# Optimization experiments

Measured on AMD Instinct MI355X. Metric: run time of the kernel, lower is better.

Reference implementation:

```python
import jax, jax.numpy as jnp
import numpy as np

N = 100000
E = 1600000
F_IN = 256   # 4 * 64 after concat
H = 128

def _glorot(key, shape):
    fan_in, fan_out = shape
    lim = jnp.sqrt(6.0 / (fan_in + fan_out))
    return jax.random.uniform(key, shape, jnp.float32, -lim, lim)

def setup_inputs() -> dict:
    key = jax.random.key(0)
    ks = jax.random.split(key, 32)
    inp = {
        'x': jax.random.normal(ks[0], (N, 64), jnp.float32),
        'diff': jax.random.normal(ks[1], (N, 64), jnp.float32),
        'rec_prev': jax.random.normal(ks[2], (N, 64), jnp.float32),
        'hidden_prev': jax.random.normal(ks[3], (N, 64), jnp.float32),
        'edge_index': jax.random.randint(ks[4], (2, E), 0, N, jnp.int64),
    }
    dims = [(F_IN, H), (H, H), (H, H), (H, 1)]
    for i, (din, dout) in enumerate(dims):
        inp[f'Wl{i}'] = _glorot(ks[5 + 3 * i], (din, dout))  # neighbor (aggr) weight
        inp[f'Wr{i}'] = _glorot(ks[6 + 3 * i], (din, dout))  # root weight
        inp[f'b{i}'] = jnp.zeros((dout,), jnp.float32)
    return inp

def _sage_conv(h, src, dst, Wl, Wr, b):
    # mean aggregation of source-node features at destination nodes (PyG SAGEConv)
    msg_sum = jax.ops.segment_sum(h[src], dst, num_segments=N)        # [N, F]
    cnt = jax.ops.segment_sum(jnp.ones((src.shape[0],), h.dtype), dst, num_segments=N)
    mean = msg_sum / jnp.maximum(cnt, 1.0)[:, None]
    return mean @ Wl + h @ Wr + b

def reference(x, diff, rec_prev, hidden_prev, edge_index,
              Wl0, Wr0, b0, Wl1, Wr1, b1, Wl2, Wr2, b2, Wl3, Wr3, b3):
    src, dst = edge_index[0], edge_index[1]
    h = jnp.concatenate([x, diff, rec_prev, hidden_prev], axis=1)  # [N, 256]
    params = [(Wl0, Wr0, b0), (Wl1, Wr1, b1), (Wl2, Wr2, b2), (Wl3, Wr3, b3)]
    h = _sage_conv(h, src, dst, *params[0])
    for Wl, Wr, b in params[1:]:
        h = jax.nn.relu(h)
        h = _sage_conv(h, src, dst, Wl, Wr, b)
    out = jax.nn.sigmoid(h)          # [N, 1]
    lwp_util = jnp.mean(out)
    return out, lwp_util
```

## Files before the change

kernel.cpp:

```cpp
#include <hip/hip_runtime.h>
#include <hip/hip_bf16.h>

#define NN 100000
#define EE 1600000
#define HH 128
#define NB 391
#define CAP 5120

typedef short bf16x8 __attribute__((ext_vector_type(8)));
typedef short bf16x4 __attribute__((ext_vector_type(4)));
typedef float f32x4  __attribute__((ext_vector_type(4)));

__device__ inline short f2bf(float v) {
    __hip_bfloat16 b = __float2bfloat16(v);
    return *reinterpret_cast<short*>(&b);
}

__global__ __launch_bounds__(512) void zerob_kernel(int* __restrict__ bcur) {
    if (threadIdx.x < NB) bcur[threadIdx.x] = 0;
}

__global__ __launch_bounds__(1024) void scatter_kernel(
    const int* __restrict__ srcv, const int* __restrict__ dstv,
    int* __restrict__ bcur, int* __restrict__ pairs) {
    __shared__ int hist[NB];
    __shared__ int base[NB];
    const int t = threadIdx.x;
    for (int j = t; j < NB; j += 1024) hist[j] = 0;
    __syncthreads();

    const int e0 = blockIdx.x * 4096;
    int s[4], d[4], n = 0;
#pragma unroll
    for (int u = 0; u < 4; ++u) {
        int e = e0 + u * 1024 + t;
        if (e < EE) { s[n] = srcv[e]; d[n] = dstv[e]; ++n; }
    }
#pragma unroll
    for (int u = 0; u < 4; ++u)
        if (u < n) atomicAdd(&hist[d[u] >> 8], 1);
    __syncthreads();

    for (int j = t; j < NB; j += 1024)
        base[j] = hist[j] ? atomicAdd(&bcur[j], hist[j]) : 0;
    __syncthreads();
    for (int j = t; j < NB; j += 1024) hist[j] = base[j];
    __syncthreads();

#pragma unroll
    for (int u = 0; u < 4; ++u)
        if (u < n) {
            const int b   = d[u] >> 8;
            const int pos = atomicAdd(&hist[b], 1);
            if (pos < CAP) pairs[b * CAP + pos] = (s[u] << 8) | (d[u] & 255);
        }
}

__global__ __launch_bounds__(256) void finalize_kernel(
    const int* __restrict__ bcur, const int* __restrict__ pairs,
    int* __restrict__ csr, int* __restrict__ beg, int* __restrict__ eend,
    float* __restrict__ inv) {
    __shared__ int cnt[256];
    __shared__ int scn[256];
    __shared__ int cur[256];
    const int b = blockIdx.x, t = threadIdx.x;
    int m = bcur[b];
    if (m > CAP) m = CAP;

    cnt[t] = 0;
    __syncthreads();
    for (int e = t; e < m; e += 256)
        atomicAdd(&cnt[pairs[b * CAP + e] & 255], 1);
    __syncthreads();

    const int v = cnt[t];
    scn[t] = v;
    __syncthreads();
    for (int st = 1; st < 256; st <<= 1) {
        int tv = (t >= st) ? scn[t - st] : 0;
        __syncthreads();
        scn[t] += tv;
        __syncthreads();
    }
    const int myStart = scn[t] - v;
    cur[t] = myStart;
    __syncthreads();

    for (int e = t; e < m; e += 256) {
        const int pk  = pairs[b * CAP + e];
        const int pos = atomicAdd(&cur[pk & 255], 1);
        csr[b * CAP + pos] = pk >> 8;
    }

    const int node = b * 256 + t;
    if (node < NN) {
        beg[node]  = b * CAP + myStart;
        eend[node] = b * CAP + myStart + v;
        inv[node]  = 1.0f / fmaxf((float)v, 1.0f);
    }
}

__global__ __launch_bounds__(256) void prepw_kernel(
    const float* __restrict__ Wl0, const float* __restrict__ Wr0,
    const float* __restrict__ Wl1, const float* __restrict__ Wr1,
    const float* __restrict__ Wl2, const float* __restrict__ Wr2,
    __hip_bfloat16* __restrict__ WT0, __hip_bfloat16* __restrict__ WT1,
    __hip_bfloat16* __restrict__ WT2) {
    int t = blockIdx.x * 256 + threadIdx.x;
    if (t < 65536) {
        int k = t & 255, n = t >> 8;
        float v = (n < 128) ? Wl0[(size_t)k * 128 + n] : Wr0[(size_t)k * 128 + (n - 128)];
        WT0[(size_t)n * 256 + k] = __float2bfloat16(v);
    } else {
        t -= 65536;
        int layer = t >> 15;
        int u = t & 32767;
        int k = u & 127, n = u >> 7;
        const float* Wl = layer ? Wl2 : Wl1;
        const float* Wr = layer ? Wr2 : Wr1;
        __hip_bfloat16* WT = layer ? WT2 : WT1;
        float v = (n < 128) ? Wl[(size_t)k * 128 + n] : Wr[(size_t)k * 128 + (n - 128)];
        WT[(size_t)n * 128 + k] = __float2bfloat16(v);
    }
}

#define TSW 136
template <int K, bool FIRST>
__global__ __launch_bounds__(256) void gemm_kernel(
    const __hip_bfloat16* hin,
    const float* __restrict__ x0, const float* __restrict__ x1,
    const float* __restrict__ x2, const float* __restrict__ x3,
    const __hip_bfloat16* __restrict__ wt, const float* __restrict__ bias,
    __hip_bfloat16* zout, __hip_bfloat16* __restrict__ rout) {
    constexpr int LDH = K + 8;
    __shared__ short lsh[2 * 64 * TSW];
    const int t    = threadIdx.x;
    const int w    = t >> 6;
    const int lane = t & 63;
    const int quad = lane >> 4;
    const int l16  = lane & 15;
    const int n0   = blockIdx.x * 64;

    if (FIRST) {
        const float* srcs[4] = {x0, x1, x2, x3};
#pragma unroll
        for (int si = 0; si < 4; ++si) {
            const float* s = srcs[si];
#pragma unroll
            for (int u = 0; u < 4; ++u) {
                const int id  = u * 256 + t;
                const int row = id >> 4, c4 = (id & 15) * 4;
                int rg = n0 + row; if (rg > NN - 1) rg = NN - 1;
                const float4 v = *(const float4*)&s[(size_t)rg * 64 + c4];
                bf16x4 p;
                p[0] = f2bf(v.x); p[1] = f2bf(v.y);
                p[2] = f2bf(v.z); p[3] = f2bf(v.w);
                *(bf16x4*)&lsh[row * LDH + si * 64 + c4] = p;
            }
        }
    } else {
        constexpr int CPR = K / 8;
#pragma unroll
        for (int u = 0; u < (64 * CPR) / 256; ++u) {
            const int id  = u * 256 + t;
            const int row = id / CPR, c8 = (id % CPR) * 8;
            int rg = n0 + row; if (rg > NN - 1) rg = NN - 1;
            const bf16x8 v = *(const bf16x8*)&hin[(size_t)rg * K + c8];
            *(bf16x8*)&lsh[row * LDH + c8] = v;
        }
    }
    __syncthreads();

    const __hip_bfloat16* afeat[4];
#pragma unroll
    for (int ft = 0; ft < 4; ++ft)
        afeat[ft] = wt + (size_t)(w * 64 + ft * 16 + l16) * K + quad * 8;

    f32x4 acc[4][4];
#pragma unroll
    for (int ft = 0; ft < 4; ++ft)
#pragma unroll
        for (int nt = 0; nt < 4; ++nt)
            acc[ft][nt] = (f32x4){0.f, 0.f, 0.f, 0.f};

#pragma unroll
    for (int kc = 0; kc < K / 32; ++kc) {
        bf16x8 af[4];
#pragma unroll
        for (int ft = 0; ft < 4; ++ft)
            af[ft] = *(const bf16x8*)(afeat[ft] + kc * 32);
        bf16x8 bf[4];
#pragma unroll
        for (int nt = 0; nt < 4; ++nt)
            bf[nt] = *(const bf16x8*)&lsh[(nt * 16 + l16) * LDH + kc * 32 + quad * 8];
#pragma unroll
        for (int ft = 0; ft < 4; ++ft)
#pragma unroll
            for (int nt = 0; nt < 4; ++nt)
                acc[ft][nt] = __builtin_amdgcn_mfma_f32_16x16x32_bf16(
                    af[ft], bf[nt], acc[ft][nt], 0, 0, 0);
    }

    __syncthreads();

    short* dstb = lsh + ((w < 2) ? 0 : 64 * TSW);
    const int fcol = (w & 1) * 64;
#pragma unroll
    for (int ft = 0; ft < 4; ++ft) {
        const int fb = ft * 16 + quad * 4;
        float4 bv = make_float4(0.f, 0.f, 0.f, 0.f);
        if (w >= 2) bv = *(const float4*)&bias[fcol + fb];
#pragma unroll
        for (int nt = 0; nt < 4; ++nt) {
            const f32x4 a = acc[ft][nt];
            bf16x4 p;
            p[0] = f2bf(a[0] + bv.x);
            p[1] = f2bf(a[1] + bv.y);
            p[2] = f2bf(a[2] + bv.z);
            p[3] = f2bf(a[3] + bv.w);
            *(bf16x4*)&dstb[(nt * 16 + l16) * TSW + fcol + fb] = p;
        }
    }
    __syncthreads();

#pragma unroll
    for (int u = 0; u < 4; ++u) {
        const int id  = u * 256 + t;
        const int row = id >> 4, ch = (id & 15) * 8;
        const int nd  = n0 + row;
        if (nd < NN) {
            const bf16x8 vz = *(const bf16x8*)&lsh[row * TSW + ch];
            *(bf16x8*)&zout[(size_t)nd * HH + ch] = vz;
            const bf16x8 vr = *(const bf16x8*)&lsh[(64 + row) * TSW + ch];
            *(bf16x8*)&rout[(size_t)nd * HH + ch] = vr;
        }
    }
}

__global__ __launch_bounds__(256) void aggregate_kernel(
    const __hip_bfloat16* __restrict__ z, __hip_bfloat16* __restrict__ rio,
    const int* __restrict__ beg, const int* __restrict__ eend,
    const int* __restrict__ csr, const float* __restrict__ inv) {
    const int i    = (blockIdx.x * 256 + threadIdx.x) >> 6;
    const int lane = threadIdx.x & 63;
    const int g    = lane >> 4;
    const int l16  = lane & 15;
    if (i >= NN) return;
    const int b0 = beg[i], e0 = eend[i];

    float acc[8];
#pragma unroll
    for (int j = 0; j < 8; ++j) acc[j] = 0.f;

    int e = b0 + g;
    for (; e + 4 < e0; e += 8) {
        const int s0 = csr[e];
        const int s1 = csr[e + 4];
        const bf16x8 z0 = *(const bf16x8*)&z[(size_t)s0 * HH + l16 * 8];
        const bf16x8 z1 = *(const bf16x8*)&z[(size_t)s1 * HH + l16 * 8];
        const __hip_bfloat162* p0 = (const __hip_bfloat162*)&z0;
        const __hip_bfloat162* p1 = (const __hip_bfloat162*)&z1;
#pragma unroll
        for (int j = 0; j < 4; ++j) {
            acc[2 * j]     += __bfloat162float(p0[j].x) + __bfloat162float(p1[j].x);
            acc[2 * j + 1] += __bfloat162float(p0[j].y) + __bfloat162float(p1[j].y);
        }
    }
    if (e < e0) {
        const int s0 = csr[e];
        const bf16x8 z0 = *(const bf16x8*)&z[(size_t)s0 * HH + l16 * 8];
        const __hip_bfloat162* p0 = (const __hip_bfloat162*)&z0;
#pragma unroll
        for (int j = 0; j < 4; ++j) {
            acc[2 * j]     += __bfloat162float(p0[j].x);
            acc[2 * j + 1] += __bfloat162float(p0[j].y);
        }
    }

#pragma unroll
    for (int j = 0; j < 8; ++j) {
        acc[j] += __shfl_xor(acc[j], 16, 64);
        acc[j] += __shfl_xor(acc[j], 32, 64);
    }

    const float iv = inv[i];
    const int   f  = l16 * 8 + g * 2;
    const __hip_bfloat162 rv = *(const __hip_bfloat162*)&rio[(size_t)i * HH + f];
    __hip_bfloat162 o;
    o.x = __float2bfloat16(fmaxf(acc[g * 2]     * iv + __bfloat162float(rv.x), 0.f));
    o.y = __float2bfloat16(fmaxf(acc[g * 2 + 1] * iv + __bfloat162float(rv.y), 0.f));
    *(__hip_bfloat162*)&rio[(size_t)i * HH + f] = o;
}

__global__ __launch_bounds__(256) void proj3_kernel(
    const __hip_bfloat16* __restrict__ h, const float* __restrict__ Wl,
    const float* __restrict__ Wr, const float* __restrict__ b,
    float* __restrict__ z3, float* __restrict__ r3) {
    const int i    = (blockIdx.x * 256 + threadIdx.x) >> 6;
    const int lane = threadIdx.x & 63;
    if (i >= NN) return;
    const __hip_bfloat162 hv = *(const __hip_bfloat162*)&h[(size_t)i * HH + lane * 2];
    const float2 wl2 = *(const float2*)&Wl[lane * 2];
    const float2 wr2 = *(const float2*)&Wr[lane * 2];
    const float hx = __bfloat162float(hv.x), hy = __bfloat162float(hv.y);
    float al = hx * wl2.x + hy * wl2.y;
    float ar = hx * wr2.x + hy * wr2.y;
#pragma unroll
    for (int m = 32; m; m >>= 1) {
        al += __shfl_xor(al, m, 64);
        ar += __shfl_xor(ar, m, 64);
    }
    if (lane == 0) {
        z3[i] = al;
        r3[i] = ar + b[0];
    }
}

__global__ __launch_bounds__(256) void final_kernel(
    const float* __restrict__ z3, const float* __restrict__ r3,
    const int* __restrict__ beg, const int* __restrict__ eend,
    const int* __restrict__ csr, const float* __restrict__ inv,
    float* __restrict__ out, float* __restrict__ partial) {
    __shared__ float red[4];
    const int i    = (blockIdx.x * 256 + threadIdx.x) >> 6;
    const int lane = threadIdx.x & 63;
    const int w    = threadIdx.x >> 6;
    float v = 0.f;
    if (i < NN) {
        const int b0 = beg[i], e0 = eend[i];
        float a = 0.f;
        for (int e = b0 + lane; e < e0; e += 64) a += z3[csr[e]];
#pragma unroll
        for (int m = 32; m; m >>= 1) a += __shfl_xor(a, m, 64);
        const float pre = a * inv[i] + r3[i];
        const float s = 1.f / (1.f + __expf(-pre));
        if (lane == 0) { out[i] = s; v = s; }
    }
    if (lane == 0) red[w] = v;
    __syncthreads();
    if (threadIdx.x == 0)
        partial[blockIdx.x] = red[0] + red[1] + red[2] + red[3];
}

__global__ __launch_bounds__(256) void mean_kernel(const float* __restrict__ partial,
                                                   int nb, float* __restrict__ out) {
    __shared__ float lds[256];
    float s = 0.f;
    for (int i = threadIdx.x; i < nb; i += 256) s += partial[i];
    lds[threadIdx.x] = s;
    __syncthreads();
    for (int st = 128; st; st >>= 1) {
        if (threadIdx.x < st) lds[threadIdx.x] += lds[threadIdx.x + st];
        __syncthreads();
    }
    if (threadIdx.x == 0) out[NN] = lds[0] / (float)NN;
}

extern "C" void kernel_launch(void* const* d_in, const int* in_sizes, int n_in,
                              void* d_out, int out_size, void* d_ws, size_t ws_size,
                              hipStream_t stream) {
    const float* x    = (const float*)d_in[0];
    const float* diff = (const float*)d_in[1];
    const float* rec  = (const float*)d_in[2];
    const float* hid  = (const float*)d_in[3];
    const int* edge   = (const int*)d_in[4];
    const int* esrc = edge;
    const int* edst = edge + EE;
    const float* Wl0 = (const float*)d_in[5];
    const float* Wr0 = (const float*)d_in[6];
    const float* b0  = (const float*)d_in[7];
    const float* Wl1 = (const float*)d_in[8];
    const float* Wr1 = (const float*)d_in[9];
    const float* b1  = (const float*)d_in[10];
    const float* Wl2 = (const float*)d_in[11];
    const float* Wr2 = (const float*)d_in[12];
    const float* b2  = (const float*)d_in[13];
    const float* Wl3 = (const float*)d_in[14];
    const float* Wr3 = (const float*)d_in[15];
    const float* b3  = (const float*)d_in[16];
    float* out = (float*)d_out;

    char* w = (char*)d_ws;
    auto alloc = [&](size_t bytes) -> void* {
        void* p = (void*)w;
        w += (bytes + 255) & ~(size_t)255;
        return p;
    };
    __hip_bfloat16* bufA = (__hip_bfloat16*)alloc((size_t)NN * HH * 2);
    __hip_bfloat16* bufB = (__hip_bfloat16*)alloc((size_t)NN * HH * 2);
    __hip_bfloat16* WT0  = (__hip_bfloat16*)alloc((size_t)256 * 256 * 2);
    __hip_bfloat16* WT1  = (__hip_bfloat16*)alloc((size_t)256 * 128 * 2);
    __hip_bfloat16* WT2  = (__hip_bfloat16*)alloc((size_t)256 * 128 * 2);
    int*   pairs   = (int*)alloc((size_t)NB * CAP * 4);
    int*   csr     = (int*)alloc((size_t)NB * CAP * 4);
    int*   bcur    = (int*)alloc((size_t)512 * 4);
    int*   beg     = (int*)alloc((size_t)NN * 4);
    int*   eend    = (int*)alloc((size_t)NN * 4);
    float* inv     = (float*)alloc((size_t)NN * 4);
    float* z3      = (float*)alloc((size_t)NN * 4);
    float* r3      = (float*)alloc((size_t)NN * 4);
    float* partial = (float*)alloc((size_t)25000 * 4);

    const int GB  = (NN + 63) / 64;
    const int WB  = (NN + 3) / 4;

    zerob_kernel<<<1, 512, 0, stream>>>(bcur);
    scatter_kernel<<<NB, 1024, 0, stream>>>(esrc, edst, bcur, pairs);
    finalize_kernel<<<NB, 256, 0, stream>>>(bcur, pairs, csr, beg, eend, inv);

    prepw_kernel<<<512, 256, 0, stream>>>(Wl0, Wr0, Wl1, Wr1, Wl2, Wr2,
                                          WT0, WT1, WT2);

    gemm_kernel<256, true><<<GB, 256, 0, stream>>>(nullptr, x, diff, rec, hid,
                                                   WT0, b0, bufA, bufB);
    aggregate_kernel<<<WB, 256, 0, stream>>>(bufA, bufB, beg, eend, csr, inv);

    gemm_kernel<128, false><<<GB, 256, 0, stream>>>(bufB, nullptr, nullptr, nullptr, nullptr,
                                                    WT1, b1, bufB, bufA);
    aggregate_kernel<<<WB, 256, 0, stream>>>(bufB, bufA, beg, eend, csr, inv);

    gemm_kernel<128, false><<<GB, 256, 0, stream>>>(bufA, nullptr, nullptr, nullptr, nullptr,
                                                    WT2, b2, bufA, bufB);
    aggregate_kernel<<<WB, 256, 0, stream>>>(bufA, bufB, beg, eend, csr, inv);

    proj3_kernel<<<WB, 256, 0, stream>>>(bufB, Wl3, Wr3, b3, z3, r3);
    final_kernel<<<WB, 256, 0, stream>>>(z3, r3, beg, eend, csr, inv, out, partial);
    mean_kernel<<<1, 256, 0, stream>>>(partial, WB, out);
}
```

Measured before the change: 553.2 us.

## Halve GEMM shared memory by staging K in 128-wide passes

The GEMM kernel now stages its input tile 128 columns at a time, looping twice for the 256-wide first layer, so the LDS buffer drops to a single 64xTSW tile. The epilogue writes the z and root outputs one after the other through that same buffer. A launch-bounds hint of 5 blocks per CU is added. The aim is higher occupancy, at the cost of extra barriers and the loss of overlap between loads and MFMA within each pass.

```diff
diff --git a/kernel.cpp b/kernel.cpp
--- a/kernel.cpp
+++ b/kernel.cpp
@@ -126,14 +126,13 @@
 
 #define TSW 136
 template <int K, bool FIRST>
-__global__ __launch_bounds__(256) void gemm_kernel(
+__global__ __launch_bounds__(256, 5) void gemm_kernel(
     const __hip_bfloat16* hin,
     const float* __restrict__ x0, const float* __restrict__ x1,
     const float* __restrict__ x2, const float* __restrict__ x3,
     const __hip_bfloat16* __restrict__ wt, const float* __restrict__ bias,
     __hip_bfloat16* zout, __hip_bfloat16* __restrict__ rout) {
-    constexpr int LDH = K + 8;
-    __shared__ short lsh[2 * 64 * TSW];
+    __shared__ short lsh[64 * TSW];
     const int t    = threadIdx.x;
     const int w    = t >> 6;
     const int lane = t & 63;
@@ -141,99 +140,118 @@
     const int l16  = lane & 15;
     const int n0   = blockIdx.x * 64;
 
-    if (FIRST) {
-        const float* srcs[4] = {x0, x1, x2, x3};
-#pragma unroll
-        for (int si = 0; si < 4; ++si) {
-            const float* s = srcs[si];
-#pragma unroll
-            for (int u = 0; u < 4; ++u) {
+    const __hip_bfloat16* afeat[4];
+#pragma unroll
+    for (int ft = 0; ft < 4; ++ft)
+        afeat[ft] = wt + (size_t)(w * 64 + ft * 16 + l16) * K + quad * 8;
+
+    f32x4 acc[4][4];
+#pragma unroll
+    for (int ft = 0; ft < 4; ++ft)
+#pragma unroll
+        for (int nt = 0; nt < 4; ++nt)
+            acc[ft][nt] = (f32x4){0.f, 0.f, 0.f, 0.f};
+
+    constexpr int NPASS = K / 128;
+#pragma unroll
+    for (int pass = 0; pass < NPASS; ++pass) {
+        if (FIRST) {
+            const float* sA = pass ? x2 : x0;
+            const float* sB = pass ? x3 : x1;
+#pragma unroll
+            for (int u = 0; u < 8; ++u) {
                 const int id  = u * 256 + t;
-                const int row = id >> 4, c4 = (id & 15) * 4;
+                const int row = id >> 5, c4 = (id & 31) * 4;
                 int rg = n0 + row; if (rg > NN - 1) rg = NN - 1;
-                const float4 v = *(const float4*)&s[(size_t)rg * 64 + c4];
+                const float* s = (c4 < 64) ? sA : sB;
+                const float4 v = *(const float4*)&s[(size_t)rg * 64 + (c4 & 63)];
                 bf16x4 p;
                 p[0] = f2bf(v.x); p[1] = f2bf(v.y);
                 p[2] = f2bf(v.z); p[3] = f2bf(v.w);
-                *(bf16x4*)&lsh[row * LDH + si * 64 + c4] = p;
+                *(bf16x4*)&lsh[row * TSW + c4] = p;
             }
-        }
-    } else {
-        constexpr int CPR = K / 8;
-#pragma unroll
-        for (int u = 0; u < (64 * CPR) / 256; ++u) {
-            const int id  = u * 256 + t;
-            const int row = id / CPR, c8 = (id % CPR) * 8;
-            int rg = n0 + row; if (rg > NN - 1) rg = NN - 1;
-            const bf16x8 v = *(const bf16x8*)&hin[(size_t)rg * K + c8];
-            *(bf16x8*)&lsh[row * LDH + c8] = v;
-        }
-    }
-    __syncthreads();
-
-    const __hip_bfloat16* afeat[4];
-#pragma unroll
-    for (int ft = 0; ft < 4; ++ft)
-        afeat[ft] = wt + (size_t)(w * 64 + ft * 16 + l16) * K + quad * 8;
-
-    f32x4 acc[4][4];
-#pragma unroll
-    for (int ft = 0; ft < 4; ++ft)
-#pragma unroll
-        for (int nt = 0; nt < 4; ++nt)
-            acc[ft][nt] = (f32x4){0.f, 0.f, 0.f, 0.f};
-
-#pragma unroll
-    for (int kc = 0; kc < K / 32; ++kc) {
-        bf16x8 af[4];
-#pragma unroll
-        for (int ft = 0; ft < 4; ++ft)
-            af[ft] = *(const bf16x8*)(afeat[ft] + kc * 32);
-        bf16x8 bf[4];
-#pragma unroll
-        for (int nt = 0; nt < 4; ++nt)
-            bf[nt] = *(const bf16x8*)&lsh[(nt * 16 + l16) * LDH + kc * 32 + quad * 8];
-#pragma unroll
-        for (int ft = 0; ft < 4; ++ft)
+        } else {
+#pragma unroll
+            for (int u = 0; u < 4; ++u) {
+                const int id  = u * 256 + t;
+                const int row = id >> 4, c8 = (id & 15) * 8;
+                int rg = n0 + row; if (rg > NN - 1) rg = NN - 1;
+                const bf16x8 v = *(const bf16x8*)&hin[(size_t)rg * K + c8];
+                *(bf16x8*)&lsh[row * TSW + c8] = v;
+            }
+        }
+        __syncthreads();
+
+#pragma unroll
+        for (int kcl = 0; kcl < 4; ++kcl) {
+            const int kc = pass * 4 + kcl;
+            bf16x8 af[4];
+#pragma unroll
+            for (int ft = 0; ft < 4; ++ft)
+                af[ft] = *(const bf16x8*)(afeat[ft] + kc * 32);
+            bf16x8 bf[4];
 #pragma unroll
             for (int nt = 0; nt < 4; ++nt)
-                acc[ft][nt] = __builtin_amdgcn_mfma_f32_16x16x32_bf16(
-                    af[ft], bf[nt], acc[ft][nt], 0, 0, 0);
-    }
-
-    __syncthreads();
-
-    short* dstb = lsh + ((w < 2) ? 0 : 64 * TSW);
-    const int fcol = (w & 1) * 64;
-#pragma unroll
-    for (int ft = 0; ft < 4; ++ft) {
-        const int fb = ft * 16 + quad * 4;
-        float4 bv = make_float4(0.f, 0.f, 0.f, 0.f);
-        if (w >= 2) bv = *(const float4*)&bias[fcol + fb];
-#pragma unroll
-        for (int nt = 0; nt < 4; ++nt) {
-            const f32x4 a = acc[ft][nt];
-            bf16x4 p;
-            p[0] = f2bf(a[0] + bv.x);
-            p[1] = f2bf(a[1] + bv.y);
-            p[2] = f2bf(a[2] + bv.z);
-            p[3] = f2bf(a[3] + bv.w);
-            *(bf16x4*)&dstb[(nt * 16 + l16) * TSW + fcol + fb] = p;
-        }
-    }
-    __syncthreads();
-
+                bf[nt] = *(const bf16x8*)&lsh[(nt * 16 + l16) * TSW + kcl * 32 + quad * 8];
+#pragma unroll
+            for (int ft = 0; ft < 4; ++ft)
+#pragma unroll
+                for (int nt = 0; nt < 4; ++nt)
+                    acc[ft][nt] = __builtin_amdgcn_mfma_f32_16x16x32_bf16(
+                        af[ft], bf[nt], acc[ft][nt], 0, 0, 0);
+        }
+        __syncthreads();
+    }
+
+    if (w < 2) {
+#pragma unroll
+        for (int ft = 0; ft < 4; ++ft) {
+            const int fb = ft * 16 + quad * 4;
+#pragma unroll
+            for (int nt = 0; nt < 4; ++nt) {
+                const f32x4 a = acc[ft][nt];
+                bf16x4 p;
+                p[0] = f2bf(a[0]); p[1] = f2bf(a[1]);
+                p[2] = f2bf(a[2]); p[3] = f2bf(a[3]);
+                *(bf16x4*)&lsh[(nt * 16 + l16) * TSW + w * 64 + fb] = p;
+            }
+        }
+    }
+    __syncthreads();
 #pragma unroll
     for (int u = 0; u < 4; ++u) {
         const int id  = u * 256 + t;
         const int row = id >> 4, ch = (id & 15) * 8;
         const int nd  = n0 + row;
-        if (nd < NN) {
-            const bf16x8 vz = *(const bf16x8*)&lsh[row * TSW + ch];
-            *(bf16x8*)&zout[(size_t)nd * HH + ch] = vz;
-            const bf16x8 vr = *(const bf16x8*)&lsh[(64 + row) * TSW + ch];
-            *(bf16x8*)&rout[(size_t)nd * HH + ch] = vr;
-        }
+        if (nd < NN)
+            *(bf16x8*)&zout[(size_t)nd * HH + ch] = *(const bf16x8*)&lsh[row * TSW + ch];
+    }
+    __syncthreads();
+
+    if (w >= 2) {
+        const int fcol = (w - 2) * 64;
+#pragma unroll
+        for (int ft = 0; ft < 4; ++ft) {
+            const int fb = ft * 16 + quad * 4;
+            const float4 bv = *(const float4*)&bias[fcol + fb];
+#pragma unroll
+            for (int nt = 0; nt < 4; ++nt) {
+                const f32x4 a = acc[ft][nt];
+                bf16x4 p;
+                p[0] = f2bf(a[0] + bv.x); p[1] = f2bf(a[1] + bv.y);
+                p[2] = f2bf(a[2] + bv.z); p[3] = f2bf(a[3] + bv.w);
+                *(bf16x4*)&lsh[(nt * 16 + l16) * TSW + fcol + fb] = p;
+            }
+        }
+    }
+    __syncthreads();
+#pragma unroll
+    for (int u = 0; u < 4; ++u) {
+        const int id  = u * 256 + t;
+        const int row = id >> 4, ch = (id & 15) * 8;
+        const int nd  = n0 + row;
+        if (nd < NN)
+            *(bf16x8*)&rout[(size_t)nd * HH + ch] = *(const bf16x8*)&lsh[row * TSW + ch];
     }
 }
 
```

New measurement: 636.8 us. +15.1%, slower.
